# Kernel tuning notes

Hardware: AMD Instinct MI355X
Metric: run time of the kernel (lower is better)

Reference implementation:

```python
import jax, jax.numpy as jnp
import numpy as np

EPS = 1e-5

def _layernorm(x):
    # elementwise_affine=False LayerNorm over last dim
    mu = jnp.mean(x, axis=-1, keepdims=True)
    var = jnp.mean(jnp.square(x - mu), axis=-1, keepdims=True)
    return (x - mu) / jnp.sqrt(var + EPS)

def setup_inputs() -> dict:
    key = jax.random.key(0)
    B, I, H = 16384, 512, 512
    ks = jax.random.split(key, 10)
    std = 1.0 / np.sqrt(H)
    u = lambda k, shape: jax.random.uniform(k, shape, jnp.float32, -std, std)
    return {
        "x": jax.random.normal(ks[0], (B, I), jnp.float32),
        "h": jax.random.normal(ks[1], (B, H), jnp.float32),
        "W_i2h": u(ks[2], (2 * H, I)),
        "b_i2h": u(ks[3], (2 * H,)),
        "W_h2h": u(ks[4], (2 * H, H)),
        "b_h2h": u(ks[5], (2 * H,)),
        "W_hatW": u(ks[6], (H, I)),
        "b_hatW": u(ks[7], (H,)),
        "W_hatU": u(ks[8], (H, H)),
        "b_hatU": u(ks[9], (H,)),
    }

def reference(x, h, W_i2h, b_i2h, W_h2h, b_h2h, W_hatW, b_hatW, W_hatU, b_hatU):
    H = W_hatU.shape[0]
    i2h = _layernorm(x @ W_i2h.T + b_i2h)   # [B, 2H]
    h2h = _layernorm(h @ W_h2h.T + b_h2h)   # [B, 2H]
    gates = jax.nn.sigmoid(i2h + h2h)
    z_t = gates[:, :H]
    r_t = gates[:, -H:]
    h_hat_a = _layernorm(x @ W_hatW.T + b_hatW)
    h_hat_b = _layernorm(h @ W_hatU.T + b_hatU)
    h_hat = jnp.tanh(h_hat_a + r_t * h_hat_b)
    h_t = (1.0 - z_t) * h + z_t * h_hat
    return h_t
```

## Files before the change

### kernel.cpp

```cpp
#include <hip/hip_runtime.h>
#include <hip/hip_bf16.h>


using f32x4 = __attribute__((ext_vector_type(4))) float;
using s16x8 = __attribute__((ext_vector_type(8))) short;
typedef __attribute__((ext_vector_type(8))) unsigned short u16x8;

#define WB_OFF   0ull
#define GB_OFF   1572864ull

__device__ __forceinline__ void async_load16(const void* g, void* l) {
  __builtin_amdgcn_global_load_lds(
      (const __attribute__((address_space(1))) unsigned int*)g,
      (__attribute__((address_space(3))) unsigned int*)l, 16, 0, 0);
}

__device__ __forceinline__ float bfraw2f(unsigned short u) {
  union { unsigned int i; float f; } c;
  c.i = ((unsigned int)u) << 16;
  return c.f;
}

__global__ __launch_bounds__(256) void convert_w_kernel(
    const float* __restrict__ w0, const float* __restrict__ w1,
    const float* __restrict__ w2, const float* __restrict__ w3,
    __hip_bfloat16* __restrict__ dst)
{
  const size_t i = (size_t)blockIdx.x * 256 + threadIdx.x;
  const float* src;
  __hip_bfloat16* d;
  size_t o;
  if (i < 131072ull)      { src = w0; d = dst;            o = i; }
  else if (i < 262144ull) { src = w1; d = dst + 524288;   o = i - 131072ull; }
  else if (i < 327680ull) { src = w2; d = dst + 1048576;  o = i - 262144ull; }
  else                    { src = w3; d = dst + 1310720;  o = i - 327680ull; }
  const float4 v = *(const float4*)(src + 4 * o);
  __hip_bfloat16 t4[4] = {__float2bfloat16(v.x), __float2bfloat16(v.y),
                          __float2bfloat16(v.z), __float2bfloat16(v.w)};
  *(uint2*)(d + 4 * o) = *(const uint2*)t4;
}


#define B_BASE 131072

__device__ __forceinline__ void stage_B_shared(const char* base, char* slot,
                                               int koff, int wave, int lane) {
#pragma unroll
  for (int i = 0; i < 2; ++i) {
    const int c = wave * 2 + i;
    const int row  = c * 16 + (lane >> 2);
    const int colb = ((lane & 3) * 16) ^ (((lane >> 3) & 3) << 4);
    async_load16(base + (size_t)row * 1024 + koff + colb,
                 slot + c * 1024 + lane * 16);
  }
}

__device__ __forceinline__ void cvt_write8(void* dst, const float4& f0,
                                           const float4& f1) {
  union { s16x8 v; __hip_bfloat16 b[8]; } u;
  u.b[0] = __float2bfloat16(f0.x); u.b[1] = __float2bfloat16(f0.y);
  u.b[2] = __float2bfloat16(f0.z); u.b[3] = __float2bfloat16(f0.w);
  u.b[4] = __float2bfloat16(f1.x); u.b[5] = __float2bfloat16(f1.y);
  u.b[6] = __float2bfloat16(f1.z); u.b[7] = __float2bfloat16(f1.w);
  *(s16x8*)dst = u.v;
}

__global__ __launch_bounds__(512, 2) void gemm_kernel(
    const float* __restrict__ xf,
    const float* __restrict__ hf,
    const __hip_bfloat16* __restrict__ Wb,
    __hip_bfloat16* __restrict__ G)
{
  const int bid   = blockIdx.x;
  const int type  = bid & 1;
  const int mband = bid >> 1;
  const int m0    = mband * 128;
  const float* Af = (type ? hf : xf) + (size_t)m0 * 512;

  __shared__ __align__(16) char lds[163840];

  const int tid  = threadIdx.x;
  const int lane = tid & 63;
  const int wave = tid >> 6;

  const int lk  = (lane >> 4) * 16;
  const int lr  = lane & 15;
  const int rdk = lk ^ (((lr >> 1) & 3) << 4);

  auto rdA = [&](int kt, int fm) {
    return *(const s16x8*)(lds + kt * 8192 + (fm * 16 + lr) * 64 + rdk);
  };
  auto rdB0 = [&](int slot, int fn) {
    return *(const s16x8*)(lds + B_BASE + slot * 16384 +
                           (wave * 32 + fn * 16 + lr) * 64 + rdk);
  };

  const int ntl0 = type ? 4 : 0;
  const char* Bb0 = (const char*)Wb + (size_t)ntl0 * 256 * 1024;

  stage_B_shared(Bb0, lds + B_BASE, 0, wave, lane);

  const int arow = tid >> 2;
  const int alin = (tid & 3) * 16;
  const int acb  = alin ^ (((arow >> 1) & 3) << 4);
  const float* abase = Af + (size_t)arow * 512 + (alin >> 1);
  char* const awr = lds + arow * 64 + acb;

  float4 hA, hB;
  {
    const float4 a0 = *(const float4*)(abase);
    const float4 a1 = *(const float4*)(abase + 4);
    hA = *(const float4*)(abase + 32);
    hB = *(const float4*)(abase + 36);
    cvt_write8(awr, a0, a1);
  }

  {
    f32x4 acc[8][2];
#pragma unroll
    for (int a = 0; a < 8; ++a)
#pragma unroll
      for (int b = 0; b < 2; ++b) acc[a][b] = (f32x4){0.f, 0.f, 0.f, 0.f};

#pragma unroll
    for (int kt = 0; kt < 16; ++kt) {
      asm volatile("s_waitcnt vmcnt(0) lgkmcnt(0)" ::: "memory");
      __builtin_amdgcn_s_barrier();

      if (kt <= 14) cvt_write8(awr + (kt + 1) * 8192, hA, hB);

      const int slot = kt & 1;
      s16x8 b[2], a[8];
#pragma unroll
      for (int fn = 0; fn < 2; ++fn) b[fn] = rdB0(slot, fn);
#pragma unroll
      for (int fm = 0; fm < 8; ++fm) a[fm] = rdA(kt, fm);

      if (kt < 15)
        stage_B_shared(Bb0, lds + B_BASE + ((kt + 1) & 1) * 16384,
                       (kt + 1) * 64, wave, lane);

      if (kt <= 13) {
        hA = *(const float4*)(abase + (kt + 2) * 32);
        hB = *(const float4*)(abase + (kt + 2) * 32 + 4);
      }

      __builtin_amdgcn_s_setprio(1);
#pragma unroll
      for (int fm = 0; fm < 8; ++fm)
#pragma unroll
        for (int fn = 0; fn < 2; ++fn)
          acc[fm][fn] = __builtin_amdgcn_mfma_f32_16x16x32_bf16(
              a[fm], b[fn], acc[fm][fn], 0, 0, 0);
      __builtin_amdgcn_s_setprio(0);
    }

    const int n0 = ntl0 * 256;
    const int mbase = m0 + ((lane >> 4) << 2);
    const int nbase = n0 + wave * 32 + lr;
#pragma unroll
    for (int fm = 0; fm < 8; ++fm)
#pragma unroll
      for (int fn = 0; fn < 2; ++fn)
#pragma unroll
        for (int r = 0; r < 4; ++r)
          G[(size_t)(mbase + fm * 16 + r) * 3072 + nbase + fn * 16] =
              __float2bfloat16(acc[fm][fn][r]);
  }

  __builtin_amdgcn_s_barrier();

  char* const pB = lds + B_BASE + wave * 4096;
  const char* const wpriv0 = (const char*)Wb + (size_t)wave * 32768;

  auto rdBp = [&](int slot, int fn) {
    return *(const s16x8*)(pB + slot * 2048 + (fn * 16 + lr) * 64 + rdk);
  };
  auto stage_Bp = [&](int ntl, int kt, int slot) {
    const char* wb = wpriv0 + (size_t)ntl * 262144;
#pragma unroll
    for (int ii = 0; ii < 2; ++ii) {
      const int row  = ii * 16 + (lane >> 2);
      const int colb = ((lane & 3) * 16) ^ (((lane >> 3) & 3) << 4);
      async_load16(wb + (size_t)row * 1024 + kt * 64 + colb,
                   pB + slot * 2048 + ii * 1024 + lane * 16);
    }
  };

  {
    const int ntl1 = type ? 5 : 1;
    stage_Bp(ntl1, 0, 0);
    stage_Bp(ntl1, 1, 1);
  }

  for (int ip = 1; ip < 6; ++ip) {
    const int ntl  = (ip < 4) ? (type ? ip + 4 : ip) : (type ? ip + 6 : ip + 4);
    const int ipn  = ip + 1;
    const int ntlN = (ip < 5) ? ((ipn < 4) ? (type ? ipn + 4 : ipn)
                                           : (type ? ipn + 6 : ipn + 4)) : ntl;

    f32x4 acc[8][2];
#pragma unroll
    for (int a = 0; a < 8; ++a)
#pragma unroll
      for (int b = 0; b < 2; ++b) acc[a][b] = (f32x4){0.f, 0.f, 0.f, 0.f};

#pragma unroll
    for (int kt = 0; kt < 16; ++kt) {
      if (ip == 5 && kt == 15) asm volatile("s_waitcnt vmcnt(0)" ::: "memory");
      else                     asm volatile("s_waitcnt vmcnt(2)" ::: "memory");

      const int slot = kt & 1;
      s16x8 b[2], a[8];
#pragma unroll
      for (int fn = 0; fn < 2; ++fn) b[fn] = rdBp(slot, fn);
#pragma unroll
      for (int fm = 0; fm < 8; ++fm) a[fm] = rdA(kt, fm);

      asm volatile("s_waitcnt lgkmcnt(0)" ::: "memory");
      __builtin_amdgcn_sched_barrier(0);
      if (kt <= 13)    stage_Bp(ntl, kt + 2, slot);
      else if (ip < 5) stage_Bp(ntlN, kt - 14, slot);

      __builtin_amdgcn_s_setprio(1);
#pragma unroll
      for (int fm = 0; fm < 8; ++fm)
#pragma unroll
        for (int fn = 0; fn < 2; ++fn)
          acc[fm][fn] = __builtin_amdgcn_mfma_f32_16x16x32_bf16(
              a[fm], b[fn], acc[fm][fn], 0, 0, 0);
      __builtin_amdgcn_s_setprio(0);
    }

    const int n0 = ntl * 256;
    const int mbase = m0 + ((lane >> 4) << 2);
    const int nbase = n0 + wave * 32 + lr;
#pragma unroll
    for (int fm = 0; fm < 8; ++fm)
#pragma unroll
      for (int fn = 0; fn < 2; ++fn)
#pragma unroll
        for (int r = 0; r < 4; ++r)
          G[(size_t)(mbase + fm * 16 + r) * 3072 + nbase + fn * 16] =
              __float2bfloat16(acc[fm][fn][r]);
  }
}

__global__ __launch_bounds__(256) void ln_gate_kernel(
    const __hip_bfloat16* __restrict__ G, const float* __restrict__ h,
    const float* __restrict__ b0, const float* __restrict__ b1,
    const float* __restrict__ b2, const float* __restrict__ b3,
    float* __restrict__ out)
{
  const int w = threadIdx.x >> 6;
  const int L = threadIdx.x & 63;
  const int row = blockIdx.x * 4 + w;
  const unsigned short* g = (const unsigned short*)(G + (size_t)row * 3072);

  __shared__ float zr[4][1024];
  float* const zw = zr[w];

  float v0[16], v1[16];
  {
    const u16x8 a0 = *(const u16x8*)(g + 16 * L);
    const u16x8 a1 = *(const u16x8*)(g + 16 * L + 8);
    const u16x8 c0 = *(const u16x8*)(g + 1024 + 16 * L);
    const u16x8 c1 = *(const u16x8*)(g + 1024 + 16 * L + 8);
#pragma unroll
    for (int q = 0; q < 4; ++q) {
      const float4 f0 = *(const float4*)(b0 + 16 * L + 4 * q);
      const float4 f1 = *(const float4*)(b1 + 16 * L + 4 * q);
      const float bb0[4] = {f0.x, f0.y, f0.z, f0.w};
      const float bb1[4] = {f1.x, f1.y, f1.z, f1.w};
#pragma unroll
      for (int j = 0; j < 4; ++j) {
        const int k = 4 * q + j;
        const unsigned short ua = (k < 8) ? a0[k] : a1[k - 8];
        const unsigned short uc = (k < 8) ? c0[k] : c1[k - 8];
        v0[k] = bfraw2f(ua) + bb0[j];
        v1[k] = bfraw2f(uc) + bb1[j];
      }
    }
  }
  float4 s = make_float4(0.f, 0.f, 0.f, 0.f);
#pragma unroll
  for (int k = 0; k < 16; ++k) {
    s.x += v0[k]; s.y += v0[k] * v0[k];
    s.z += v1[k]; s.w += v1[k] * v1[k];
  }
#pragma unroll
  for (int off = 1; off < 64; off <<= 1) {
    s.x += __shfl_xor(s.x, off);
    s.y += __shfl_xor(s.y, off);
    s.z += __shfl_xor(s.z, off);
    s.w += __shfl_xor(s.w, off);
  }
  const float mu0 = s.x * (1.f / 1024.f);
  const float mu1 = s.z * (1.f / 1024.f);
  const float rs0 = rsqrtf(s.y * (1.f / 1024.f) - mu0 * mu0 + 1e-5f);
  const float rs1 = rsqrtf(s.w * (1.f / 1024.f) - mu1 * mu1 + 1e-5f);

#pragma unroll
  for (int k = 0; k < 16; ++k) {
    const float pre = (v0[k] - mu0) * rs0 + (v1[k] - mu1) * rs1;
    zw[k * 64 + L] = 1.f / (1.f + __expf(-pre));
  }

  float v2[8], v3[8];
  {
    const u16x8 a = *(const u16x8*)(g + 2048 + 8 * L);
    const u16x8 c = *(const u16x8*)(g + 2560 + 8 * L);
#pragma unroll
    for (int q = 0; q < 2; ++q) {
      const float4 f2 = *(const float4*)(b2 + 8 * L + 4 * q);
      const float4 f3 = *(const float4*)(b3 + 8 * L + 4 * q);
      const float bb2[4] = {f2.x, f2.y, f2.z, f2.w};
      const float bb3[4] = {f3.x, f3.y, f3.z, f3.w};
#pragma unroll
      for (int j = 0; j < 4; ++j) {
        const int k = 4 * q + j;
        v2[k] = bfraw2f(a[k]) + bb2[j];
        v3[k] = bfraw2f(c[k]) + bb3[j];
      }
    }
  }
  float4 t = make_float4(0.f, 0.f, 0.f, 0.f);
#pragma unroll
  for (int k = 0; k < 8; ++k) {
    t.x += v2[k]; t.y += v2[k] * v2[k];
    t.z += v3[k]; t.w += v3[k] * v3[k];
  }
#pragma unroll
  for (int off = 1; off < 64; off <<= 1) {
    t.x += __shfl_xor(t.x, off);
    t.y += __shfl_xor(t.y, off);
    t.z += __shfl_xor(t.z, off);
    t.w += __shfl_xor(t.w, off);
  }
  const float mu2 = t.x * (1.f / 512.f);
  const float mu3 = t.z * (1.f / 512.f);
  const float rs2 = rsqrtf(t.y * (1.f / 512.f) - mu2 * mu2 + 1e-5f);
  const float rs3 = rsqrtf(t.w * (1.f / 512.f) - mu3 * mu3 + 1e-5f);

  asm volatile("s_waitcnt lgkmcnt(0)" ::: "memory");

  const float4 h0 = *(const float4*)(h + (size_t)row * 512 + 8 * L);
  const float4 h1 = *(const float4*)(h + (size_t)row * 512 + 8 * L + 4);
  const float hv[8] = {h0.x, h0.y, h0.z, h0.w, h1.x, h1.y, h1.z, h1.w};

  float o[8];
#pragma unroll
  for (int k = 0; k < 8; ++k) {
    const int c  = 8 * L + k;
    const float z  = zw[(c & 15) * 64 + (c >> 4)];
    const float rr = zw[((512 + c) & 15) * 64 + ((512 + c) >> 4)];
    const float ha  = (v2[k] - mu2) * rs2;
    const float hbv = (v3[k] - mu3) * rs3;
    const float hhat = tanhf(ha + rr * hbv);
    o[k] = (1.f - z) * hv[k] + z * hhat;
  }
  *(float4*)(out + (size_t)row * 512 + 8 * L)     = make_float4(o[0], o[1], o[2], o[3]);
  *(float4*)(out + (size_t)row * 512 + 8 * L + 4) = make_float4(o[4], o[5], o[6], o[7]);
}

extern "C" void kernel_launch(void* const* d_in, const int* in_sizes, int n_in,
                              void* d_out, int out_size, void* d_ws, size_t ws_size,
                              hipStream_t stream) {
  (void)in_sizes; (void)n_in; (void)out_size; (void)ws_size;
  const float* x      = (const float*)d_in[0];
  const float* h      = (const float*)d_in[1];
  const float* W_i2h  = (const float*)d_in[2];
  const float* b_i2h  = (const float*)d_in[3];
  const float* W_h2h  = (const float*)d_in[4];
  const float* b_h2h  = (const float*)d_in[5];
  const float* W_hatW = (const float*)d_in[6];
  const float* b_hatW = (const float*)d_in[7];
  const float* W_hatU = (const float*)d_in[8];
  const float* b_hatU = (const float*)d_in[9];
  float* out = (float*)d_out;
  __hip_bfloat16* ws = (__hip_bfloat16*)d_ws;

  convert_w_kernel<<<1536, 256, 0, stream>>>(W_i2h, W_h2h, W_hatW, W_hatU,
                                             ws + WB_OFF);
  gemm_kernel<<<256, 512, 0, stream>>>(x, h, ws + WB_OFF, ws + GB_OFF);
  ln_gate_kernel<<<4096, 256, 0, stream>>>(ws + GB_OFF, h, b_i2h, b_h2h,
                                           b_hatW, b_hatU, out);
}
```

Baseline: 97.94 us.

## Double GEMM block to 16 waves, each computing 16-column N slices

Launches the fused GEMM with 1024 threads so each wave computes a 128x16 tile instead of 128x32. The per-wave B staging and private B double buffers are halved, and only the first 512 threads convert and stage the fp32 A tile. This increases wave-level parallelism and cuts per-wave accumulator registers, but each A fragment read from LDS now feeds only one MFMA, doubling A LDS traffic. The block-wide barriers also now synchronise twice as many waves.

```diff
diff --git a/kernel.cpp b/kernel.cpp
--- a/kernel.cpp
+++ b/kernel.cpp
@@ -43,18 +43,6 @@
 
 #define B_BASE 131072
 
-__device__ __forceinline__ void stage_B_shared(const char* base, char* slot,
-                                               int koff, int wave, int lane) {
-#pragma unroll
-  for (int i = 0; i < 2; ++i) {
-    const int c = wave * 2 + i;
-    const int row  = c * 16 + (lane >> 2);
-    const int colb = ((lane & 3) * 16) ^ (((lane >> 3) & 3) << 4);
-    async_load16(base + (size_t)row * 1024 + koff + colb,
-                 slot + c * 1024 + lane * 16);
-  }
-}
-
 __device__ __forceinline__ void cvt_write8(void* dst, const float4& f0,
                                            const float4& f1) {
   union { s16x8 v; __hip_bfloat16 b[8]; } u;
@@ -65,7 +53,7 @@
   *(s16x8*)dst = u.v;
 }
 
-__global__ __launch_bounds__(512, 2) void gemm_kernel(
+__global__ __launch_bounds__(1024, 4) void gemm_kernel(
     const float* __restrict__ xf,
     const float* __restrict__ hf,
     const __hip_bfloat16* __restrict__ Wb,
@@ -90,24 +78,31 @@
   auto rdA = [&](int kt, int fm) {
     return *(const s16x8*)(lds + kt * 8192 + (fm * 16 + lr) * 64 + rdk);
   };
-  auto rdB0 = [&](int slot, int fn) {
+  auto rdB0 = [&](int slot) {
     return *(const s16x8*)(lds + B_BASE + slot * 16384 +
-                           (wave * 32 + fn * 16 + lr) * 64 + rdk);
+                           (wave * 16 + lr) * 64 + rdk);
+  };
+  auto stage_B_shared = [&](const char* base, char* slot, int koff) {
+    const int row  = wave * 16 + (lane >> 2);
+    const int colb = ((lane & 3) * 16) ^ (((lane >> 3) & 3) << 4);
+    async_load16(base + (size_t)row * 1024 + koff + colb,
+                 slot + wave * 1024 + lane * 16);
   };
 
   const int ntl0 = type ? 4 : 0;
   const char* Bb0 = (const char*)Wb + (size_t)ntl0 * 256 * 1024;
 
-  stage_B_shared(Bb0, lds + B_BASE, 0, wave, lane);
-
-  const int arow = tid >> 2;
+  stage_B_shared(Bb0, lds + B_BASE, 0);
+
+  const int arow = (tid & 511) >> 2;
   const int alin = (tid & 3) * 16;
   const int acb  = alin ^ (((arow >> 1) & 3) << 4);
   const float* abase = Af + (size_t)arow * 512 + (alin >> 1);
   char* const awr = lds + arow * 64 + acb;
+  const bool athread = (tid < 512);
 
   float4 hA, hB;
-  {
+  if (athread) {
     const float4 a0 = *(const float4*)(abase);
     const float4 a1 = *(const float4*)(abase + 4);
     hA = *(const float4*)(abase + 32);
@@ -116,31 +111,29 @@
   }
 
   {
-    f32x4 acc[8][2];
-#pragma unroll
-    for (int a = 0; a < 8; ++a)
-#pragma unroll
-      for (int b = 0; b < 2; ++b) acc[a][b] = (f32x4){0.f, 0.f, 0.f, 0.f};
+    f32x4 acc[8];
+#pragma unroll
+    for (int a = 0; a < 8; ++a) acc[a] = (f32x4){0.f, 0.f, 0.f, 0.f};
 
 #pragma unroll
     for (int kt = 0; kt < 16; ++kt) {
       asm volatile("s_waitcnt vmcnt(0) lgkmcnt(0)" ::: "memory");
       __builtin_amdgcn_s_barrier();
 
-      if (kt <= 14) cvt_write8(awr + (kt + 1) * 8192, hA, hB);
+      if (athread && kt <= 14)
+        cvt_write8(awr + (kt + 1) * 8192, hA, hB);
 
       const int slot = kt & 1;
-      s16x8 b[2], a[8];
-#pragma unroll
-      for (int fn = 0; fn < 2; ++fn) b[fn] = rdB0(slot, fn);
+      s16x8 a[8];
+      const s16x8 b = rdB0(slot);
 #pragma unroll
       for (int fm = 0; fm < 8; ++fm) a[fm] = rdA(kt, fm);
 
       if (kt < 15)
         stage_B_shared(Bb0, lds + B_BASE + ((kt + 1) & 1) * 16384,
-                       (kt + 1) * 64, wave, lane);
-
-      if (kt <= 13) {
+                       (kt + 1) * 64);
+
+      if (athread && kt <= 13) {
         hA = *(const float4*)(abase + (kt + 2) * 32);
         hB = *(const float4*)(abase + (kt + 2) * 32 + 4);
       }
@@ -148,43 +141,36 @@
       __builtin_amdgcn_s_setprio(1);
 #pragma unroll
       for (int fm = 0; fm < 8; ++fm)
-#pragma unroll
-        for (int fn = 0; fn < 2; ++fn)
-          acc[fm][fn] = __builtin_amdgcn_mfma_f32_16x16x32_bf16(
-              a[fm], b[fn], acc[fm][fn], 0, 0, 0);
+        acc[fm] = __builtin_amdgcn_mfma_f32_16x16x32_bf16(a[fm], b, acc[fm],
+                                                          0, 0, 0);
       __builtin_amdgcn_s_setprio(0);
     }
 
     const int n0 = ntl0 * 256;
     const int mbase = m0 + ((lane >> 4) << 2);
-    const int nbase = n0 + wave * 32 + lr;
+    const int nn = n0 + wave * 16 + lr;
 #pragma unroll
     for (int fm = 0; fm < 8; ++fm)
 #pragma unroll
-      for (int fn = 0; fn < 2; ++fn)
-#pragma unroll
-        for (int r = 0; r < 4; ++r)
-          G[(size_t)(mbase + fm * 16 + r) * 3072 + nbase + fn * 16] =
-              __float2bfloat16(acc[fm][fn][r]);
+      for (int r = 0; r < 4; ++r)
+        G[(size_t)(mbase + fm * 16 + r) * 3072 + nn] =
+            __float2bfloat16(acc[fm][r]);
   }
 
   __builtin_amdgcn_s_barrier();
 
-  char* const pB = lds + B_BASE + wave * 4096;
-  const char* const wpriv0 = (const char*)Wb + (size_t)wave * 32768;
-
-  auto rdBp = [&](int slot, int fn) {
-    return *(const s16x8*)(pB + slot * 2048 + (fn * 16 + lr) * 64 + rdk);
+  char* const pB = lds + B_BASE + wave * 2048;
+  const char* const wpriv0 = (const char*)Wb + (size_t)wave * 16384;
+
+  auto rdBp = [&](int slot) {
+    return *(const s16x8*)(pB + slot * 1024 + lr * 64 + rdk);
   };
   auto stage_Bp = [&](int ntl, int kt, int slot) {
     const char* wb = wpriv0 + (size_t)ntl * 262144;
-#pragma unroll
-    for (int ii = 0; ii < 2; ++ii) {
-      const int row  = ii * 16 + (lane >> 2);
-      const int colb = ((lane & 3) * 16) ^ (((lane >> 3) & 3) << 4);
-      async_load16(wb + (size_t)row * 1024 + kt * 64 + colb,
-                   pB + slot * 2048 + ii * 1024 + lane * 16);
-    }
+    const int row  = lane >> 2;
+    const int colb = ((lane & 3) * 16) ^ (((lane >> 3) & 3) << 4);
+    async_load16(wb + (size_t)row * 1024 + kt * 64 + colb,
+                 pB + slot * 1024 + lane * 16);
   };
 
   {
@@ -199,21 +185,18 @@
     const int ntlN = (ip < 5) ? ((ipn < 4) ? (type ? ipn + 4 : ipn)
                                            : (type ? ipn + 6 : ipn + 4)) : ntl;
 
-    f32x4 acc[8][2];
-#pragma unroll
-    for (int a = 0; a < 8; ++a)
-#pragma unroll
-      for (int b = 0; b < 2; ++b) acc[a][b] = (f32x4){0.f, 0.f, 0.f, 0.f};
+    f32x4 acc[8];
+#pragma unroll
+    for (int a = 0; a < 8; ++a) acc[a] = (f32x4){0.f, 0.f, 0.f, 0.f};
 
 #pragma unroll
     for (int kt = 0; kt < 16; ++kt) {
       if (ip == 5 && kt == 15) asm volatile("s_waitcnt vmcnt(0)" ::: "memory");
-      else                     asm volatile("s_waitcnt vmcnt(2)" ::: "memory");
+      else                     asm volatile("s_waitcnt vmcnt(1)" ::: "memory");
 
       const int slot = kt & 1;
-      s16x8 b[2], a[8];
-#pragma unroll
-      for (int fn = 0; fn < 2; ++fn) b[fn] = rdBp(slot, fn);
+      const s16x8 b = rdBp(slot);
+      s16x8 a[8];
 #pragma unroll
       for (int fm = 0; fm < 8; ++fm) a[fm] = rdA(kt, fm);
 
@@ -225,24 +208,20 @@
       __builtin_amdgcn_s_setprio(1);
 #pragma unroll
       for (int fm = 0; fm < 8; ++fm)
-#pragma unroll
-        for (int fn = 0; fn < 2; ++fn)
-          acc[fm][fn] = __builtin_amdgcn_mfma_f32_16x16x32_bf16(
-              a[fm], b[fn], acc[fm][fn], 0, 0, 0);
+        acc[fm] = __builtin_amdgcn_mfma_f32_16x16x32_bf16(a[fm], b, acc[fm],
+                                                          0, 0, 0);
       __builtin_amdgcn_s_setprio(0);
     }
 
     const int n0 = ntl * 256;
     const int mbase = m0 + ((lane >> 4) << 2);
-    const int nbase = n0 + wave * 32 + lr;
+    const int nn = n0 + wave * 16 + lr;
 #pragma unroll
     for (int fm = 0; fm < 8; ++fm)
 #pragma unroll
-      for (int fn = 0; fn < 2; ++fn)
-#pragma unroll
-        for (int r = 0; r < 4; ++r)
-          G[(size_t)(mbase + fm * 16 + r) * 3072 + nbase + fn * 16] =
-              __float2bfloat16(acc[fm][fn][r]);
+      for (int r = 0; r < 4; ++r)
+        G[(size_t)(mbase + fm * 16 + r) * 3072 + nn] =
+            __float2bfloat16(acc[fm][r]);
   }
 }
 
@@ -382,7 +361,7 @@
 
   convert_w_kernel<<<1536, 256, 0, stream>>>(W_i2h, W_h2h, W_hatW, W_hatU,
                                              ws + WB_OFF);
-  gemm_kernel<<<256, 512, 0, stream>>>(x, h, ws + WB_OFF, ws + GB_OFF);
+  gemm_kernel<<<256, 1024, 0, stream>>>(x, h, ws + WB_OFF, ws + GB_OFF);
   ln_gate_kernel<<<4096, 256, 0, stream>>>(ws + GB_OFF, h, b_i2h, b_h2h,
                                            b_hatW, b_hatU, out);
 }
```

New measurement: 161.9 us. 65.3% more time.
